# Optimization experiments

Measured on AMD Instinct MI355X. Metric: run time of the kernel, lower is better.

Reference implementation:

```python
import jax, jax.numpy as jnp
import numpy as np

MODES = 16

def setup_inputs() -> dict:
    key = jax.random.key(0)
    k1, k2 = jax.random.split(key)
    x = jax.random.normal(k1, (16, 32, 256, 256), dtype=jnp.float32)
    weights = jax.random.normal(k2, (32, 32, MODES, MODES, 2), dtype=jnp.float32) * 0.1
    return {"x": x, "weights": weights}

def reference(x, weights):
    # x: [B, Ci, H, W]; weights: [Ci, Co, m, m, 2]
    B, Ci, H, W = x.shape
    m = weights.shape[2]
    Co = weights.shape[1]
    x_ft = jnp.fft.rfft2(x, axes=(-2, -1))  # [B, Ci, H, W//2+1] complex
    w_c = jax.lax.complex(weights[..., 0], weights[..., 1])  # [Ci, Co, m, m]
    low = jnp.einsum('bixy,ioxy->boxy', x_ft[:, :, :m, :m], w_c)  # [B, Co, m, m]
    out_ft = jnp.zeros((B, Co, H, W // 2 + 1), dtype=x_ft.dtype)
    out_ft = out_ft.at[:, :, :m, :m].set(low)
    return jnp.fft.irfft2(out_ft, s=(H, W), axes=(-2, -1)).astype(x.dtype)
```

## Files before the change

kernel.cpp:

```cpp
#include <hip/hip_runtime.h>

typedef float v4 __attribute__((ext_vector_type(4)));
typedef float f32x4 __attribute__((ext_vector_type(4)));
typedef short bf16x8 __attribute__((ext_vector_type(8)));

#define TWO_PI_256 0.024543692606170259f


__device__ __forceinline__ unsigned short f2bf(float f) {
  const unsigned int u = __float_as_uint(f);
  return (unsigned short)((u + 0x7fffu + ((u >> 16) & 1u)) >> 16);
}
__device__ __forceinline__ float bf2f(unsigned short h) {
  return __uint_as_float(((unsigned int)h) << 16);
}

__global__ __launch_bounds__(256) void k0_trig(unsigned short* __restrict__ Th,
                                               unsigned short* __restrict__ Tl,
                                               unsigned short* __restrict__ Bh,
                                               unsigned short* __restrict__ Bl) {
  const int k = threadIdx.x;
#pragma unroll
  for (int kx = 0; kx < 16; ++kx) {
    float sv, cv;
    sincosf((float)((kx * k) & 255) * TWO_PI_256, &sv, &cv);
    const float vals[2] = {cv, -sv};
#pragma unroll
    for (int p = 0; p < 2; ++p) {
      const int o = 2 * kx + p;
      const unsigned short hi = f2bf(vals[p]);
      Th[o * 256 + k] = hi;
      Tl[o * 256 + k] = f2bf(vals[p] - bf2f(hi));
    }
  }
  for (int idx = threadIdx.x; idx < 8192; idx += 256) {
    const int nt = idx >> 9;
    const int lane = (idx >> 3) & 63;
    const int j = idx & 7;
    const int q = lane >> 4;
    const int n16 = lane & 15;
    const int kk = q * 8 + j;
    const int w = nt * 16 + n16;
    float val;
    if (kk == 0) {
      val = 1.f / 65536.f;
    } else if (kk == 16) {
      val = 0.f;
    } else {
      const int kx = kk & 15;
      float sv, cv;
      sincosf((float)((kx * w) & 255) * TWO_PI_256, &sv, &cv);
      val = (kk < 16 ? 2.f * cv : -2.f * sv) * (1.f / 65536.f);
    }
    const unsigned short hi = f2bf(val);
    Bh[idx] = hi;
    Bl[idx] = f2bf(val - bf2f(hi));
  }
}

typedef __attribute__((address_space(1))) const unsigned int gas_u32;
typedef __attribute__((address_space(3))) unsigned int las_u32;

__global__ __launch_bounds__(256) void k1_dftw(const float* __restrict__ x,
                                               const unsigned short* __restrict__ Th,
                                               const unsigned short* __restrict__ Tl,
                                               float* __restrict__ F) {
  __shared__ float Xs[128 * 32];
  __shared__ __align__(16) unsigned short Ts[2][32 * 264];
  const int tid = threadIdx.x;
  const int lane = tid & 63;
  const int w = tid >> 6;
  const long rblk = (long)blockIdx.x * 128;
  {
    const int o = tid >> 3, kb = (tid & 7) * 32;
#pragma unroll
    for (int f = 0; f < 2; ++f) {
      const unsigned short* src = (f ? Tl : Th) + o * 256 + kb;
      unsigned short* dst = &Ts[f][o * 264 + kb];
#pragma unroll
      for (int j = 0; j < 32; j += 8)
        *(bf16x8*)(dst + j) = *(const bf16x8*)(src + j);
    }
  }
  const int q = lane >> 4;
  const int n16 = lane & 15;
  f32x4 acc[2][2] = {};
  for (int kc = 0; kc < 256; kc += 32) {
    __syncthreads();
#pragma unroll
    for (int i = 0; i < 4; ++i) {
      const int r0 = w * 32 + i * 8;
      __builtin_amdgcn_global_load_lds(
          (gas_u32*)(x + (rblk + r0 + (lane >> 3)) * 256 + kc + (lane & 7) * 4),
          (las_u32*)((unsigned int*)Xs + r0 * 32), 16, 0, 0);
    }
    __syncthreads();
    bf16x8 bh[2], bl[2];
#pragma unroll
    for (int nt = 0; nt < 2; ++nt) {
      const int o = nt * 16 + n16;
      bh[nt] = *(const bf16x8*)&Ts[0][o * 264 + kc + q * 8];
      bl[nt] = *(const bf16x8*)&Ts[1][o * 264 + kc + q * 8];
    }
#pragma unroll
    for (int mt = 0; mt < 2; ++mt) {
      const int m = w * 32 + mt * 16 + n16;
      const float* ap = &Xs[m * 32 + q * 8];
      const v4 a0 = *(const v4*)ap;
      const v4 a1 = *(const v4*)(ap + 4);
      const float af[8] = {a0[0], a0[1], a0[2], a0[3], a1[0], a1[1], a1[2], a1[3]};
      bf16x8 ah, al;
#pragma unroll
      for (int j = 0; j < 8; ++j) {
        const unsigned short h = f2bf(af[j]);
        ah[j] = (short)h;
        al[j] = (short)f2bf(af[j] - bf2f(h));
      }
#pragma unroll
      for (int nt = 0; nt < 2; ++nt) {
        acc[mt][nt] = __builtin_amdgcn_mfma_f32_16x16x32_bf16(ah, bh[nt], acc[mt][nt], 0, 0, 0);
        acc[mt][nt] = __builtin_amdgcn_mfma_f32_16x16x32_bf16(al, bh[nt], acc[mt][nt], 0, 0, 0);
        acc[mt][nt] = __builtin_amdgcn_mfma_f32_16x16x32_bf16(ah, bl[nt], acc[mt][nt], 0, 0, 0);
      }
    }
  }
#pragma unroll
  for (int mt = 0; mt < 2; ++mt)
#pragma unroll
    for (int nt = 0; nt < 2; ++nt)
#pragma unroll
      for (int r = 0; r < 4; ++r) {
        const long row = rblk + w * 32 + mt * 16 + q * 4 + r;
        F[row * 32 + nt * 16 + n16] = acc[mt][nt][r];
      }
}

__global__ __launch_bounds__(256) void k2_dfth(const float* __restrict__ F,
                                               float* __restrict__ X) {
  __shared__ float2 tbl[256];
  __shared__ float Fs[64][36];
  const int tid = threadIdx.x;
  const int bc = blockIdx.x;
  {
    float sv, cv;
    sincosf((float)tid * TWO_PI_256, &sv, &cv);
    tbl[tid] = make_float2(cv, sv);
  }
  const int kx = tid & 15;
  const int ky = tid >> 4;
  float xr = 0.f, xi = 0.f;
  const float* Fb = F + (long)bc * 8192;
  for (int hc = 0; hc < 256; hc += 64) {
    __syncthreads();
#pragma unroll
    for (int p = 0; p < 2; ++p) {
      const int h = (tid >> 3) + p * 32;
      const int j = (tid & 7) * 4;
      *(v4*)&Fs[h][j] = *(const v4*)&Fb[(hc + h) * 32 + j];
    }
    __syncthreads();
#pragma unroll 8
    for (int hl = 0; hl < 64; ++hl) {
      const int h = hc + hl;
      const float2 f = *(const float2*)&Fs[hl][2 * kx];
      const float2 w = tbl[(ky * h) & 255];
      xr += f.x * w.x + f.y * w.y;
      xi += f.y * w.x - f.x * w.y;
    }
  }
  *(float2*)&X[((long)bc * 256 + tid) * 2] = make_float2(xr, xi);
}

__global__ __launch_bounds__(256) void k3_mix(const float* __restrict__ X,
                                              const float* __restrict__ Wt,
                                              float* __restrict__ Y) {
  const int t = threadIdx.x;
  const int co = blockIdx.x;
  const int b = blockIdx.y;
  float yr = 0.f, yi = 0.f;
#pragma unroll 4
  for (int ci = 0; ci < 32; ++ci) {
    const float2 xv = *(const float2*)&X[((long)(b * 32 + ci) * 256 + t) * 2];
    const float2 wv = *(const float2*)&Wt[((long)(ci * 32 + co) * 256 + t) * 2];
    yr += xv.x * wv.x - xv.y * wv.y;
    yi += xv.x * wv.y + xv.y * wv.x;
  }
  *(float2*)&Y[((long)(b * 32 + co) * 256 + t) * 2] = make_float2(yr, yi);
}

__global__ __launch_bounds__(256) void k4_inv(const float* __restrict__ Y,
                                              const unsigned short* __restrict__ Bh,
                                              const unsigned short* __restrict__ Bl,
                                              float* __restrict__ out) {
  __shared__ float2 tbl[256];
  __shared__ float2 Ys[256];
  __shared__ float Gs[128][36];
  const int tid = threadIdx.x;
  const int lane = tid & 63;
  const int wv = tid >> 6;
  const int co = blockIdx.x >> 1;
  const int h0 = (blockIdx.x & 1) << 7;
  const int b = blockIdx.y;
  const long bc = b * 32 + co;
  {
    float sv, cv;
    sincosf((float)tid * TWO_PI_256, &sv, &cv);
    tbl[tid] = make_float2(cv, sv);
  }
  Ys[tid] = *(const float2*)&Y[(bc * 256 + tid) * 2];
  __syncthreads();
  {
    const int hl = tid >> 1;
    const int p = tid & 1;
    const int h = h0 + hl;
    float gr[8] = {}, gi[8] = {};
#pragma unroll 4
    for (int ky = 0; ky < 16; ++ky) {
      const float2 wt = tbl[(ky * h) & 255];
#pragma unroll
      for (int i = 0; i < 8; ++i) {
        const float2 yv = Ys[ky * 16 + p * 8 + i];
        gr[i] += yv.x * wt.x - yv.y * wt.y;
        gi[i] += yv.x * wt.y + yv.y * wt.x;
      }
    }
#pragma unroll
    for (int i = 0; i < 8; ++i) {
      const int kx = p * 8 + i;
      Gs[hl][kx] = gr[i];
      Gs[hl][16 + kx] = gi[i];
    }
  }
  __syncthreads();
  const int q = lane >> 4;
  const int n16 = lane & 15;
  bf16x8 ah[2], al[2];
#pragma unroll
  for (int mt = 0; mt < 2; ++mt) {
    const float* ap = &Gs[wv * 32 + mt * 16 + n16][q * 8];
    const v4 a0 = *(const v4*)ap;
    const v4 a1 = *(const v4*)(ap + 4);
    const float af[8] = {a0[0], a0[1], a0[2], a0[3], a1[0], a1[1], a1[2], a1[3]};
#pragma unroll
    for (int j = 0; j < 8; ++j) {
      const unsigned short hh = f2bf(af[j]);
      ah[mt][j] = (short)hh;
      al[mt][j] = (short)f2bf(af[j] - bf2f(hh));
    }
  }
  f32x4 acc[2][16] = {};
#pragma unroll
  for (int nt = 0; nt < 16; ++nt) {
    const bf16x8 bhf = *(const bf16x8*)&Bh[(nt * 64 + lane) * 8];
    const bf16x8 blf = *(const bf16x8*)&Bl[(nt * 64 + lane) * 8];
#pragma unroll
    for (int mt = 0; mt < 2; ++mt) {
      acc[mt][nt] = __builtin_amdgcn_mfma_f32_16x16x32_bf16(ah[mt], bhf, acc[mt][nt], 0, 0, 0);
      acc[mt][nt] = __builtin_amdgcn_mfma_f32_16x16x32_bf16(al[mt], bhf, acc[mt][nt], 0, 0, 0);
      acc[mt][nt] = __builtin_amdgcn_mfma_f32_16x16x32_bf16(ah[mt], blf, acc[mt][nt], 0, 0, 0);
    }
  }
  float* __restrict__ ob = out + bc * 65536;
#pragma unroll
  for (int mt = 0; mt < 2; ++mt)
#pragma unroll
    for (int r = 0; r < 4; ++r) {
      const int h = h0 + wv * 32 + mt * 16 + q * 4 + r;
#pragma unroll
      for (int nt = 0; nt < 16; ++nt)
        ob[h * 256 + nt * 16 + n16] = acc[mt][nt][r];
    }
}

extern "C" void kernel_launch(void* const* d_in, const int* in_sizes, int n_in,
                              void* d_out, int out_size, void* d_ws, size_t ws_size,
                              hipStream_t stream) {
  const float* x = (const float*)d_in[0];
  const float* wt = (const float*)d_in[1];
  float* out = (float*)d_out;
  float* F = (float*)d_ws;
  float* X = F + 4194304;
  float* Yv = X + 262144;
  unsigned short* Th = (unsigned short*)(Yv + 262144);
  unsigned short* Tl = Th + 8192;
  unsigned short* Bh = Tl + 8192;
  unsigned short* Bl = Bh + 8192;
  k0_trig<<<1, 256, 0, stream>>>(Th, Tl, Bh, Bl);
  k1_dftw<<<1024, 256, 0, stream>>>(x, Th, Tl, F);
  k2_dfth<<<512, 256, 0, stream>>>(F, X);
  k3_mix<<<dim3(32, 16), 256, 0, stream>>>(X, wt, Yv);
  k4_inv<<<dim3(64, 16), 256, 0, stream>>>(Yv, Bh, Bl, out);
}
```

Measured before the change: 303.2 us.

## Fuse channel mixing into inverse kernel, parallelize trig setup, use recurrence twiddles

Result: faster. 295.4 us (-2.6%).

```diff
diff --git a/kernel.cpp b/kernel.cpp
--- a/kernel.cpp
+++ b/kernel.cpp
@@ -20,20 +20,18 @@
                                                unsigned short* __restrict__ Bh,
                                                unsigned short* __restrict__ Bl) {
   const int k = threadIdx.x;
-#pragma unroll
-  for (int kx = 0; kx < 16; ++kx) {
+  const int o = blockIdx.x;
+  {
+    const int kx = o >> 1, p = o & 1;
     float sv, cv;
     sincosf((float)((kx * k) & 255) * TWO_PI_256, &sv, &cv);
-    const float vals[2] = {cv, -sv};
-#pragma unroll
-    for (int p = 0; p < 2; ++p) {
-      const int o = 2 * kx + p;
-      const unsigned short hi = f2bf(vals[p]);
-      Th[o * 256 + k] = hi;
-      Tl[o * 256 + k] = f2bf(vals[p] - bf2f(hi));
-    }
-  }
-  for (int idx = threadIdx.x; idx < 8192; idx += 256) {
+    const float val = p ? -sv : cv;
+    const unsigned short hi = f2bf(val);
+    Th[o * 256 + k] = hi;
+    Tl[o * 256 + k] = f2bf(val - bf2f(hi));
+  }
+  {
+    const int idx = o * 256 + k;
     const int nt = idx >> 9;
     const int lane = (idx >> 3) & 63;
     const int j = idx & 7;
@@ -137,17 +135,14 @@
 
 __global__ __launch_bounds__(256) void k2_dfth(const float* __restrict__ F,
                                                float* __restrict__ X) {
-  __shared__ float2 tbl[256];
   __shared__ float Fs[64][36];
   const int tid = threadIdx.x;
   const int bc = blockIdx.x;
-  {
-    float sv, cv;
-    sincosf((float)tid * TWO_PI_256, &sv, &cv);
-    tbl[tid] = make_float2(cv, sv);
-  }
   const int kx = tid & 15;
   const int ky = tid >> 4;
+  float sn, cs;
+  sincosf((float)ky * TWO_PI_256, &sn, &cs);
+  float wr = 1.f, wi = 0.f;
   float xr = 0.f, xi = 0.f;
   const float* Fb = F + (long)bc * 8192;
   for (int hc = 0; hc < 256; hc += 64) {
@@ -161,37 +156,23 @@
     __syncthreads();
 #pragma unroll 8
     for (int hl = 0; hl < 64; ++hl) {
-      const int h = hc + hl;
       const float2 f = *(const float2*)&Fs[hl][2 * kx];
-      const float2 w = tbl[(ky * h) & 255];
-      xr += f.x * w.x + f.y * w.y;
-      xi += f.y * w.x - f.x * w.y;
+      xr += f.x * wr + f.y * wi;
+      xi += f.y * wr - f.x * wi;
+      const float nwr = wr * cs - wi * sn;
+      const float nwi = wr * sn + wi * cs;
+      wr = nwr;
+      wi = nwi;
     }
   }
   *(float2*)&X[((long)bc * 256 + tid) * 2] = make_float2(xr, xi);
 }
 
-__global__ __launch_bounds__(256) void k3_mix(const float* __restrict__ X,
-                                              const float* __restrict__ Wt,
-                                              float* __restrict__ Y) {
-  const int t = threadIdx.x;
-  const int co = blockIdx.x;
-  const int b = blockIdx.y;
-  float yr = 0.f, yi = 0.f;
-#pragma unroll 4
-  for (int ci = 0; ci < 32; ++ci) {
-    const float2 xv = *(const float2*)&X[((long)(b * 32 + ci) * 256 + t) * 2];
-    const float2 wv = *(const float2*)&Wt[((long)(ci * 32 + co) * 256 + t) * 2];
-    yr += xv.x * wv.x - xv.y * wv.y;
-    yi += xv.x * wv.y + xv.y * wv.x;
-  }
-  *(float2*)&Y[((long)(b * 32 + co) * 256 + t) * 2] = make_float2(yr, yi);
-}
-
-__global__ __launch_bounds__(256) void k4_inv(const float* __restrict__ Y,
-                                              const unsigned short* __restrict__ Bh,
-                                              const unsigned short* __restrict__ Bl,
-                                              float* __restrict__ out) {
+__global__ __launch_bounds__(256) void kB_mixinv(const float* __restrict__ X,
+                                                 const float* __restrict__ Wt,
+                                                 const unsigned short* __restrict__ Bh,
+                                                 const unsigned short* __restrict__ Bl,
+                                                 float* __restrict__ out) {
   __shared__ float2 tbl[256];
   __shared__ float2 Ys[256];
   __shared__ float Gs[128][36];
@@ -207,7 +188,19 @@
     sincosf((float)tid * TWO_PI_256, &sv, &cv);
     tbl[tid] = make_float2(cv, sv);
   }
-  Ys[tid] = *(const float2*)&Y[(bc * 256 + tid) * 2];
+  {
+    float yr = 0.f, yi = 0.f;
+    const float2* Xb = (const float2*)X + (long)b * 8192 + tid;
+    const float2* Wb = (const float2*)Wt + (long)co * 256 + tid;
+#pragma unroll 8
+    for (int ci = 0; ci < 32; ++ci) {
+      const float2 xv = Xb[ci * 256];
+      const float2 wv2 = Wb[ci * 8192];
+      yr += xv.x * wv2.x - xv.y * wv2.y;
+      yi += xv.x * wv2.y + xv.y * wv2.x;
+    }
+    Ys[tid] = make_float2(yr, yi);
+  }
   __syncthreads();
   {
     const int hl = tid >> 1;
@@ -280,14 +273,12 @@
   float* out = (float*)d_out;
   float* F = (float*)d_ws;
   float* X = F + 4194304;
-  float* Yv = X + 262144;
-  unsigned short* Th = (unsigned short*)(Yv + 262144);
+  unsigned short* Th = (unsigned short*)(X + 262144);
   unsigned short* Tl = Th + 8192;
   unsigned short* Bh = Tl + 8192;
   unsigned short* Bl = Bh + 8192;
-  k0_trig<<<1, 256, 0, stream>>>(Th, Tl, Bh, Bl);
+  k0_trig<<<32, 256, 0, stream>>>(Th, Tl, Bh, Bl);
   k1_dftw<<<1024, 256, 0, stream>>>(x, Th, Tl, F);
   k2_dfth<<<512, 256, 0, stream>>>(F, X);
-  k3_mix<<<dim3(32, 16), 256, 0, stream>>>(X, wt, Yv);
-  k4_inv<<<dim3(64, 16), 256, 0, stream>>>(Yv, Bh, Bl, out);
-}
+  kB_mixinv<<<dim3(64, 16), 256, 0, stream>>>(X, wt, Bh, Bl, out);
+}
```
